# Optimization experiments

Hardware: AMD Instinct MI355X
Metric: run time of the kernel (lower is better)

The kernel has to match this reference:

```python
import jax, jax.numpy as jnp
import numpy as np

N, E, P, D = 100000, 800000, 100000, 128

def setup_inputs() -> dict:
    key = jax.random.key(0)
    ks = jax.random.split(key, 24)
    def w(k, i, o):
        return jax.random.normal(k, (i, o), jnp.float32) * (1.0 / np.sqrt(i))
    inp = {
        'x': jax.random.normal(ks[0], (N, D), jnp.float32),
        'src': jax.random.randint(ks[1], (E,), 0, N, jnp.int32),
        'dst': jax.random.randint(ks[2], (E,), 0, N, jnp.int32),
        'pos_src': jax.random.randint(ks[3], (P,), 0, N, jnp.int32),
        'pos_dst': jax.random.randint(ks[4], (P,), 0, N, jnp.int32),
        'neg_src': jax.random.randint(ks[5], (P,), 0, N, jnp.int32),
        'neg_dst': jax.random.randint(ks[6], (P,), 0, N, jnp.int32),
        # SAGEConv params: fc_self, fc_neigh (+bias) per layer
        'Ws0': w(ks[7], D, D), 'Wn0': w(ks[8], D, D), 'b0': jnp.zeros((D,), jnp.float32),
        'Ws1': w(ks[9], D, D), 'Wn1': w(ks[10], D, D), 'b1': jnp.zeros((D,), jnp.float32),
        'Ws2': w(ks[11], D, D), 'Wn2': w(ks[12], D, D), 'b2': jnp.zeros((D,), jnp.float32),
        # predictor MLP: D->D->D->2
        'Wp0': w(ks[13], D, D), 'bp0': jnp.zeros((D,), jnp.float32),
        'Wp1': w(ks[14], D, D), 'bp1': jnp.zeros((D,), jnp.float32),
        'Wp2': w(ks[15], D, 2), 'bp2': jnp.zeros((2,), jnp.float32),
    }
    return inp

def _sage_layer(h, src, dst, n, Ws, Wn, b, act):
    # mean aggregation over in-neighbors (gather -> segment_sum -> divide)
    msum = jax.ops.segment_sum(h[src], dst, num_segments=n)      # [N, D]
    deg = jax.ops.segment_sum(jnp.ones_like(dst, jnp.float32), dst, num_segments=n)
    h_neigh = msum / jnp.maximum(deg, 1.0)[:, None]
    out = h @ Ws + h_neigh @ Wn + b
    return jax.nn.relu(out) if act else out

def _predict(hs, hd, Wp0, bp0, Wp1, bp1, Wp2, bp2):
    z = hs * hd
    z = jax.nn.relu(z @ Wp0 + bp0)
    z = jax.nn.relu(z @ Wp1 + bp1)
    return jax.nn.softmax(z @ Wp2 + bp2, axis=1)[:, 1]

def reference(x, src, dst, pos_src, pos_dst, neg_src, neg_dst,
              Ws0, Wn0, b0, Ws1, Wn1, b1, Ws2, Wn2, b2,
              Wp0, bp0, Wp1, bp1, Wp2, bp2):
    n = x.shape[0]
    h = _sage_layer(x, src, dst, n, Ws0, Wn0, b0, True)
    h = _sage_layer(h, src, dst, n, Ws1, Wn1, b1, True)
    h = _sage_layer(h, src, dst, n, Ws2, Wn2, b2, False)
    pos = _predict(h[pos_src], h[pos_dst], Wp0, bp0, Wp1, bp1, Wp2, bp2)
    neg = _predict(h[neg_src], h[neg_dst], Wp0, bp0, Wp1, bp1, Wp2, bp2)
    return (pos, neg)
```

## Files before the change

### kernel.cpp

```cpp
#include <hip/hip_runtime.h>
#include <cstdint>
#include <cstddef>
#include <cmath>

#define D 128

typedef short bf16x8 __attribute__((ext_vector_type(8)));
typedef float f32x4 __attribute__((ext_vector_type(4)));

__device__ __forceinline__ ushort f2b(float f) {
  uint x = __float_as_uint(f);
  uint r = ((x >> 16) & 1u) + 0x7fffu;
  return (ushort)((x + r) >> 16);
}
__device__ __forceinline__ float b2f(ushort u) {
  return __uint_as_float(((uint)u) << 16);
}

__global__ void k_degree(const int* __restrict__ dst, int E, int* __restrict__ deg) {
  int e = blockIdx.x * blockDim.x + threadIdx.x;
  if (e < E) atomicAdd(&deg[dst[e]], 1);
}

#define SCAN_T 256
#define SCAN_E 4
#define SCAN_CHUNK (SCAN_T * SCAN_E)

__global__ void k_scan_partial(const int* __restrict__ deg, int n, int* __restrict__ part) {
  __shared__ int s[SCAN_T];
  int base = blockIdx.x * SCAN_CHUNK;
  int sum = 0;
  for (int i = 0; i < SCAN_E; ++i) {
    int idx = base + (int)threadIdx.x * SCAN_E + i;
    if (idx < n) sum += deg[idx];
  }
  s[threadIdx.x] = sum; __syncthreads();
  for (int ofs = SCAN_T / 2; ofs > 0; ofs >>= 1) {
    if ((int)threadIdx.x < ofs) s[threadIdx.x] += s[threadIdx.x + ofs];
    __syncthreads();
  }
  if (threadIdx.x == 0) part[blockIdx.x] = s[0];
}

__global__ void k_scan_part_ex(int* __restrict__ part, int nb) {
  __shared__ int s[1024];
  int v = ((int)threadIdx.x < nb) ? part[threadIdx.x] : 0;
  s[threadIdx.x] = v; __syncthreads();
  for (int ofs = 1; ofs < 1024; ofs <<= 1) {
    int t = ((int)threadIdx.x >= ofs) ? s[threadIdx.x - ofs] : 0;
    __syncthreads();
    s[threadIdx.x] += t;
    __syncthreads();
  }
  if ((int)threadIdx.x < nb) part[threadIdx.x] = s[threadIdx.x] - v;
}

__global__ void k_scan_final(const int* __restrict__ deg, int n, const int* __restrict__ part,
                             int* __restrict__ rowptr, int E) {
  __shared__ int s[SCAN_T];
  int base = blockIdx.x * SCAN_CHUNK;
  int v[SCAN_E]; int local = 0;
  for (int i = 0; i < SCAN_E; ++i) {
    int idx = base + (int)threadIdx.x * SCAN_E + i;
    v[i] = (idx < n) ? deg[idx] : 0;
    local += v[i];
  }
  s[threadIdx.x] = local; __syncthreads();
  for (int ofs = 1; ofs < SCAN_T; ofs <<= 1) {
    int t = ((int)threadIdx.x >= ofs) ? s[threadIdx.x - ofs] : 0;
    __syncthreads();
    s[threadIdx.x] += t;
    __syncthreads();
  }
  int run = part[blockIdx.x] + s[threadIdx.x] - local;
  for (int i = 0; i < SCAN_E; ++i) {
    int idx = base + (int)threadIdx.x * SCAN_E + i;
    if (idx < n) rowptr[idx] = run;
    run += v[i];
  }
  if (blockIdx.x == 0 && threadIdx.x == 0) rowptr[n] = E;
}

__global__ void k_fill(const int* __restrict__ src, const int* __restrict__ dst, int E,
                       int* __restrict__ cursor, int* __restrict__ csrc) {
  int e = blockIdx.x * blockDim.x + threadIdx.x;
  if (e < E) {
    int p = atomicAdd(&cursor[dst[e]], 1);
    csrc[p] = src[e];
  }
}

__global__ void k_conv_bf16(const float* __restrict__ in, ushort* __restrict__ out, int n8) {
  int i = blockIdx.x * 256 + threadIdx.x;
  if (i >= n8) return;
  float4 a = ((const float4*)in)[i * 2];
  float4 b = ((const float4*)in)[i * 2 + 1];
  ushort4 o0 = {f2b(a.x), f2b(a.y), f2b(a.z), f2b(a.w)};
  ushort4 o1 = {f2b(b.x), f2b(b.y), f2b(b.z), f2b(b.w)};
  ((ushort4*)out)[i * 2] = o0;
  ((ushort4*)out)[i * 2 + 1] = o1;
}

__global__ void k_packW(const float* __restrict__ W0, const float* __restrict__ W1,
                        ushort* __restrict__ out, int ksteps) {
  int o = blockIdx.x * 256 + threadIdx.x;
  int total = ksteps * 4096;
  if (o >= total) return;
  int j = o & 7, lane = (o >> 3) & 63, t = (o >> 9) & 7, ks = o >> 12;
  int k = ks * 32 + ((lane >> 4) * 8) + j;
  int n = t * 16 + (lane & 15);
  const float* W = (k < 128) ? W0 : W1;
  int kk = (k < 128) ? k : k - 128;
  out[o] = f2b(W[(size_t)kk * D + n]);
}

__global__ __launch_bounds__(256) void k_aggregate_b(const ushort* __restrict__ h,
    const int* __restrict__ rowptr, const int* __restrict__ csrc,
    ushort* __restrict__ hn, int N) {
  int wid = (int)((blockIdx.x * (size_t)blockDim.x + threadIdx.x) >> 6);
  int lane = threadIdx.x & 63;
  if (wid >= N) return;
  int grp = lane >> 4, sub = lane & 15;
  int beg = rowptr[wid], end = rowptr[wid + 1];
  const ushort* hb = h + sub * 8;
  float f[8] = {0.f, 0.f, 0.f, 0.f, 0.f, 0.f, 0.f, 0.f};
  int i = beg + grp;
  for (; i + 4 < end; i += 8) {
    int s0 = csrc[i], s1 = csrc[i + 4];
    bf16x8 v0 = *(const bf16x8*)(hb + (size_t)s0 * D);
    bf16x8 v1 = *(const bf16x8*)(hb + (size_t)s1 * D);
    #pragma unroll
    for (int j = 0; j < 8; ++j)
      f[j] += b2f((ushort)v0[j]) + b2f((ushort)v1[j]);
  }
  if (i < end) {
    int s0 = csrc[i];
    bf16x8 v0 = *(const bf16x8*)(hb + (size_t)s0 * D);
    #pragma unroll
    for (int j = 0; j < 8; ++j) f[j] += b2f((ushort)v0[j]);
  }
  #pragma unroll
  for (int j = 0; j < 8; ++j) {
    f[j] += __shfl_xor(f[j], 16);
    f[j] += __shfl_xor(f[j], 32);
  }
  if (grp == 0) {
    float inv = (end > beg) ? (1.0f / (float)(end - beg)) : 0.0f;
    bf16x8 o;
    #pragma unroll
    for (int j = 0; j < 8; ++j) o[j] = (short)f2b(f[j] * inv);
    *(bf16x8*)(hn + (size_t)wid * D + sub * 8) = o;
  }
}

__global__ __launch_bounds__(256) void k_gemm_mfma(
    const ushort* __restrict__ A, const ushort* __restrict__ An,
    const ushort* __restrict__ Bp, const float* __restrict__ bias,
    ushort* __restrict__ out, int N, int do_relu) {
  int tid = threadIdx.x;
  int wave = tid >> 6, lane = tid & 63;
  int m = lane & 15, kg = lane >> 4;
  int row0 = blockIdx.x * 64 + wave * 16;
  int ar = row0 + m; if (ar >= N) ar = N - 1;
  const ushort* a_self = A  + (size_t)ar * D + kg * 8;
  const ushort* a_nei  = An + (size_t)ar * D + kg * 8;
  f32x4 acc[8];
  #pragma unroll
  for (int t = 0; t < 8; ++t) acc[t] = f32x4{0.f, 0.f, 0.f, 0.f};
  #pragma unroll
  for (int ks = 0; ks < 8; ++ks) {
    const ushort* ap = (ks < 4) ? a_self : a_nei;
    bf16x8 af = *(const bf16x8*)(ap + (ks & 3) * 32);
    const ushort* bb = Bp + (size_t)ks * 4096 + lane * 8;
    #pragma unroll
    for (int t = 0; t < 8; ++t)
      acc[t] = __builtin_amdgcn_mfma_f32_16x16x32_bf16(af, *(const bf16x8*)(bb + t * 512), acc[t], 0, 0, 0);
  }
  #pragma unroll
  for (int t = 0; t < 8; ++t) {
    int c = t * 16 + m;
    float bv = bias[c];
    #pragma unroll
    for (int i = 0; i < 4; ++i) {
      int r = row0 + kg * 4 + i;
      float v = acc[t][i] + bv;
      if (do_relu) v = fmaxf(v, 0.f);
      if (r < N) out[(size_t)r * D + c] = f2b(v);
    }
  }
}

__global__ __launch_bounds__(256) void k_predict_mfma(
    const ushort* __restrict__ h, const int* __restrict__ sidx, const int* __restrict__ didx,
    const ushort* __restrict__ Bp0, const float* __restrict__ bp0,
    const ushort* __restrict__ Bp1, const float* __restrict__ bp1,
    const float* __restrict__ Wp2, const float* __restrict__ bp2,
    float* __restrict__ outp, int P) {
  __shared__ __align__(16) ushort z1p[4][2048];
  int tid = threadIdx.x;
  int wave = tid >> 6, lane = tid & 63;
  int m = lane & 15, kg = lane >> 4;
  int pair0 = blockIdx.x * 64 + wave * 16;
  int prow = pair0 + m; int pr = (prow < P) ? prow : P - 1;
  int si = sidx[pr], di = didx[pr];
  const ushort* hs = h + (size_t)si * D + kg * 8;
  const ushort* hd = h + (size_t)di * D + kg * 8;
  f32x4 acc[8];
  #pragma unroll
  for (int t = 0; t < 8; ++t) acc[t] = f32x4{0.f, 0.f, 0.f, 0.f};
  #pragma unroll
  for (int ks = 0; ks < 4; ++ks) {
    bf16x8 as8 = *(const bf16x8*)(hs + ks * 32);
    bf16x8 ad8 = *(const bf16x8*)(hd + ks * 32);
    bf16x8 af;
    #pragma unroll
    for (int j = 0; j < 8; ++j) {
      float p = b2f((ushort)as8[j]) * b2f((ushort)ad8[j]);
      af[j] = (short)f2b(p);
    }
    const ushort* bb = Bp0 + (size_t)ks * 4096 + lane * 8;
    #pragma unroll
    for (int t = 0; t < 8; ++t)
      acc[t] = __builtin_amdgcn_mfma_f32_16x16x32_bf16(af, *(const bf16x8*)(bb + t * 512), acc[t], 0, 0, 0);
  }
  ushort* zp = &z1p[wave][0];
  #pragma unroll
  for (int t = 0; t < 8; ++t) {
    int c = t * 16 + m;
    float bv = bp0[c];
    int ks2 = c >> 5, kg2 = (c >> 3) & 3, j2 = c & 7;
    #pragma unroll
    for (int i = 0; i < 4; ++i) {
      float v = fmaxf(acc[t][i] + bv, 0.f);
      int l2 = kg2 * 16 + kg * 4 + i;
      zp[(ks2 * 64 + l2) * 8 + j2] = f2b(v);
    }
  }
  __syncthreads();
  #pragma unroll
  for (int t = 0; t < 8; ++t) acc[t] = f32x4{0.f, 0.f, 0.f, 0.f};
  #pragma unroll
  for (int ks = 0; ks < 4; ++ks) {
    bf16x8 af = *(const bf16x8*)(zp + (ks * 64 + lane) * 8);
    const ushort* bb = Bp1 + (size_t)ks * 4096 + lane * 8;
    #pragma unroll
    for (int t = 0; t < 8; ++t)
      acc[t] = __builtin_amdgcn_mfma_f32_16x16x32_bf16(af, *(const bf16x8*)(bb + t * 512), acc[t], 0, 0, 0);
  }
  float p0[4] = {0.f, 0.f, 0.f, 0.f}, p1[4] = {0.f, 0.f, 0.f, 0.f};
  #pragma unroll
  for (int t = 0; t < 8; ++t) {
    int c = t * 16 + m;
    float bv = bp1[c];
    float wa = Wp2[(size_t)c * 2], wb = Wp2[(size_t)c * 2 + 1];
    #pragma unroll
    for (int i = 0; i < 4; ++i) {
      float z = fmaxf(acc[t][i] + bv, 0.f);
      p0[i] += z * wa;
      p1[i] += z * wb;
    }
  }
  #pragma unroll
  for (int msk = 1; msk <= 8; msk <<= 1) {
    #pragma unroll
    for (int i = 0; i < 4; ++i) {
      p0[i] += __shfl_xor(p0[i], msk);
      p1[i] += __shfl_xor(p1[i], msk);
    }
  }
  if (m == 0) {
    float c0 = bp2[0], c1 = bp2[1];
    #pragma unroll
    for (int i = 0; i < 4; ++i) {
      int r = pair0 + kg * 4 + i;
      if (r < P) {
        float l0 = p0[i] + c0, l1 = p1[i] + c1;
        outp[r] = 1.0f / (1.0f + expf(l0 - l1));
      }
    }
  }
}

extern "C" void kernel_launch(void* const* d_in, const int* in_sizes, int n_in,
                              void* d_out, int out_size, void* d_ws, size_t ws_size,
                              hipStream_t stream) {
  const float* x       = (const float*)d_in[0];
  const int*   src     = (const int*)d_in[1];
  const int*   dst     = (const int*)d_in[2];
  const int*   pos_src = (const int*)d_in[3];
  const int*   pos_dst = (const int*)d_in[4];
  const int*   neg_src = (const int*)d_in[5];
  const int*   neg_dst = (const int*)d_in[6];
  const float* Ws0 = (const float*)d_in[7],  *Wn0 = (const float*)d_in[8],  *b0 = (const float*)d_in[9];
  const float* Ws1 = (const float*)d_in[10], *Wn1 = (const float*)d_in[11], *b1 = (const float*)d_in[12];
  const float* Ws2 = (const float*)d_in[13], *Wn2 = (const float*)d_in[14], *b2 = (const float*)d_in[15];
  const float* Wp0 = (const float*)d_in[16], *bp0 = (const float*)d_in[17];
  const float* Wp1 = (const float*)d_in[18], *bp1 = (const float*)d_in[19];
  const float* Wp2 = (const float*)d_in[20], *bp2 = (const float*)d_in[21];
  const int N = in_sizes[0] / D;
  const int E = in_sizes[1];
  const int P = in_sizes[3];
  float* outp = (float*)d_out;

  char* ws = (char*)d_ws;
  size_t off = 0;
  auto alloc = [&](size_t bytes) -> void* {
    void* p = ws + off;
    off += (bytes + 255) & ~(size_t)255;
    return p;
  };
  ushort* xb    = (ushort*)alloc((size_t)N * D * 2);
  ushort* h1    = (ushort*)alloc((size_t)N * D * 2);
  ushort* h2    = (ushort*)alloc((size_t)N * D * 2);
  ushort* hn    = (ushort*)alloc((size_t)N * D * 2);
  ushort* BpL0  = (ushort*)alloc(256 * D * 2);
  ushort* BpL1  = (ushort*)alloc(256 * D * 2);
  ushort* BpL2  = (ushort*)alloc(256 * D * 2);
  ushort* BpP0  = (ushort*)alloc(128 * D * 2);
  ushort* BpP1  = (ushort*)alloc(128 * D * 2);
  int*    deg    = (int*)alloc((size_t)N * 4);
  int*    rowptr = (int*)alloc((size_t)(N + 1) * 4);
  int*    cursor = (int*)alloc((size_t)N * 4);
  int*    part   = (int*)alloc(4096);
  int*    csrc   = (int*)alloc((size_t)E * 4);
  (void)ws_size; (void)n_in; (void)out_size;

  hipMemsetAsync(deg, 0, (size_t)N * 4, stream);
  int eb = (E + 255) / 256;
  k_degree<<<eb, 256, 0, stream>>>(dst, E, deg);
  int nb = (N + SCAN_CHUNK - 1) / SCAN_CHUNK;
  k_scan_partial<<<nb, SCAN_T, 0, stream>>>(deg, N, part);
  k_scan_part_ex<<<1, 1024, 0, stream>>>(part, nb);
  k_scan_final<<<nb, SCAN_T, 0, stream>>>(deg, N, part, rowptr, E);
  hipMemcpyAsync(cursor, rowptr, (size_t)N * 4, hipMemcpyDeviceToDevice, stream);
  k_fill<<<eb, 256, 0, stream>>>(src, dst, E, cursor, csrc);

  int n8 = N * D / 8;
  k_conv_bf16<<<(n8 + 255) / 256, 256, 0, stream>>>(x, xb, n8);
  k_packW<<<(8 * 4096 + 255) / 256, 256, 0, stream>>>(Ws0, Wn0, BpL0, 8);
  k_packW<<<(8 * 4096 + 255) / 256, 256, 0, stream>>>(Ws1, Wn1, BpL1, 8);
  k_packW<<<(8 * 4096 + 255) / 256, 256, 0, stream>>>(Ws2, Wn2, BpL2, 8);
  k_packW<<<(4 * 4096 + 255) / 256, 256, 0, stream>>>(Wp0, Wp0, BpP0, 4);
  k_packW<<<(4 * 4096 + 255) / 256, 256, 0, stream>>>(Wp1, Wp1, BpP1, 4);

  int aggb = (int)(((size_t)N * 64 + 255) / 256);
  int gemb = (N + 63) / 64;
  k_aggregate_b<<<aggb, 256, 0, stream>>>(xb, rowptr, csrc, hn, N);
  k_gemm_mfma<<<gemb, 256, 0, stream>>>(xb, hn, BpL0, b0, h1, N, 1);
  k_aggregate_b<<<aggb, 256, 0, stream>>>(h1, rowptr, csrc, hn, N);
  k_gemm_mfma<<<gemb, 256, 0, stream>>>(h1, hn, BpL1, b1, h2, N, 1);
  k_aggregate_b<<<aggb, 256, 0, stream>>>(h2, rowptr, csrc, hn, N);
  k_gemm_mfma<<<gemb, 256, 0, stream>>>(h2, hn, BpL2, b2, xb, N, 0);
  int pb = (P + 63) / 64;
  k_predict_mfma<<<pb, 256, 0, stream>>>(xb, pos_src, pos_dst, BpP0, bp0, BpP1, bp1, Wp2, bp2, outp, P);
  k_predict_mfma<<<pb, 256, 0, stream>>>(xb, neg_src, neg_dst, BpP0, bp0, BpP1, bp1, Wp2, bp2, outp + P, P);
}
```

Baseline: 500.2 us.

## Fuse aggregation into SAGE GEMM, partition CSR build, merge pack and predict launches

Each SAGE layer now does its neighbor mean aggregation inside the GEMM kernel, staging the 16 mean rows per wave in shared memory. This removes the hn intermediate buffer and three extra launches. The degree and fill kernels are split into 8 destination-range partitions, with each block handling only one partition so atomics land in a narrower address range. Weight packing and the pos/neg predictions are each merged into a single launch. The costs are that every edge chunk is read 8 times during the CSR build, and the aggregation inside the fused kernel now runs at GEMM-block granularity, so occupancy and latency hiding may be lower.

```diff
diff --git a/kernel.cpp b/kernel.cpp
--- a/kernel.cpp
+++ b/kernel.cpp
@@ -17,9 +17,37 @@
   return __uint_as_float(((uint)u) << 16);
 }
 
-__global__ void k_degree(const int* __restrict__ dst, int E, int* __restrict__ deg) {
-  int e = blockIdx.x * blockDim.x + threadIdx.x;
-  if (e < E) atomicAdd(&deg[dst[e]], 1);
+__global__ __launch_bounds__(256) void k_degree_p(const int* __restrict__ dst, int E,
+    int* __restrict__ deg, float scale, int CE) {
+  int part = blockIdx.x & 7, chunk = blockIdx.x >> 3;
+  long base = (long)chunk * CE;
+  for (int i = threadIdx.x; i < CE; i += 256) {
+    long e = base + i;
+    if (e < E) {
+      int d = dst[e];
+      int p = (int)((float)d * scale); if (p > 7) p = 7;
+      if (p == part) atomicAdd(&deg[d], 1);
+    }
+  }
+}
+
+__global__ __launch_bounds__(256) void k_fill_p(const int* __restrict__ src,
+    const int* __restrict__ dst, int E, int* __restrict__ cursor,
+    int* __restrict__ csrc, float scale, int CE) {
+  int part = blockIdx.x & 7, chunk = blockIdx.x >> 3;
+  long base = (long)chunk * CE;
+  for (int i = threadIdx.x; i < CE; i += 256) {
+    long e = base + i;
+    if (e < E) {
+      int d = dst[e];
+      int p = (int)((float)d * scale); if (p > 7) p = 7;
+      if (p == part) {
+        int s = src[e];
+        int pos = atomicAdd(&cursor[d], 1);
+        csrc[pos] = s;
+      }
+    }
+  }
 }
 
 #define SCAN_T 256
@@ -81,15 +109,6 @@
   if (blockIdx.x == 0 && threadIdx.x == 0) rowptr[n] = E;
 }
 
-__global__ void k_fill(const int* __restrict__ src, const int* __restrict__ dst, int E,
-                       int* __restrict__ cursor, int* __restrict__ csrc) {
-  int e = blockIdx.x * blockDim.x + threadIdx.x;
-  if (e < E) {
-    int p = atomicAdd(&cursor[dst[e]], 1);
-    csrc[p] = src[e];
-  }
-}
-
 __global__ void k_conv_bf16(const float* __restrict__ in, ushort* __restrict__ out, int n8) {
   int i = blockIdx.x * 256 + threadIdx.x;
   if (i >= n8) return;
@@ -101,76 +120,82 @@
   ((ushort4*)out)[i * 2 + 1] = o1;
 }
 
-__global__ void k_packW(const float* __restrict__ W0, const float* __restrict__ W1,
-                        ushort* __restrict__ out, int ksteps) {
+__global__ void k_pack_all(
+    const float* __restrict__ Ws0, const float* __restrict__ Wn0,
+    const float* __restrict__ Ws1, const float* __restrict__ Wn1,
+    const float* __restrict__ Ws2, const float* __restrict__ Wn2,
+    const float* __restrict__ Wp0, const float* __restrict__ Wp1,
+    ushort* __restrict__ BpL0, ushort* __restrict__ BpL1, ushort* __restrict__ BpL2,
+    ushort* __restrict__ BpP0, ushort* __restrict__ BpP1) {
   int o = blockIdx.x * 256 + threadIdx.x;
-  int total = ksteps * 4096;
-  if (o >= total) return;
-  int j = o & 7, lane = (o >> 3) & 63, t = (o >> 9) & 7, ks = o >> 12;
+  const float *W0, *W1; ushort* out; int rel;
+  if (o < 32768)       { W0 = Ws0; W1 = Wn0; out = BpL0; rel = o; }
+  else if (o < 65536)  { W0 = Ws1; W1 = Wn1; out = BpL1; rel = o - 32768; }
+  else if (o < 98304)  { W0 = Ws2; W1 = Wn2; out = BpL2; rel = o - 65536; }
+  else if (o < 114688) { W0 = Wp0; W1 = Wp0; out = BpP0; rel = o - 98304; }
+  else                 { W0 = Wp1; W1 = Wp1; out = BpP1; rel = o - 114688; }
+  int j = rel & 7, lane = (rel >> 3) & 63, t = (rel >> 9) & 7, ks = rel >> 12;
   int k = ks * 32 + ((lane >> 4) * 8) + j;
   int n = t * 16 + (lane & 15);
   const float* W = (k < 128) ? W0 : W1;
   int kk = (k < 128) ? k : k - 128;
-  out[o] = f2b(W[(size_t)kk * D + n]);
-}
-
-__global__ __launch_bounds__(256) void k_aggregate_b(const ushort* __restrict__ h,
-    const int* __restrict__ rowptr, const int* __restrict__ csrc,
-    ushort* __restrict__ hn, int N) {
-  int wid = (int)((blockIdx.x * (size_t)blockDim.x + threadIdx.x) >> 6);
-  int lane = threadIdx.x & 63;
-  if (wid >= N) return;
-  int grp = lane >> 4, sub = lane & 15;
-  int beg = rowptr[wid], end = rowptr[wid + 1];
-  const ushort* hb = h + sub * 8;
-  float f[8] = {0.f, 0.f, 0.f, 0.f, 0.f, 0.f, 0.f, 0.f};
-  int i = beg + grp;
-  for (; i + 4 < end; i += 8) {
-    int s0 = csrc[i], s1 = csrc[i + 4];
-    bf16x8 v0 = *(const bf16x8*)(hb + (size_t)s0 * D);
-    bf16x8 v1 = *(const bf16x8*)(hb + (size_t)s1 * D);
-    #pragma unroll
-    for (int j = 0; j < 8; ++j)
-      f[j] += b2f((ushort)v0[j]) + b2f((ushort)v1[j]);
-  }
-  if (i < end) {
-    int s0 = csrc[i];
-    bf16x8 v0 = *(const bf16x8*)(hb + (size_t)s0 * D);
-    #pragma unroll
-    for (int j = 0; j < 8; ++j) f[j] += b2f((ushort)v0[j]);
-  }
-  #pragma unroll
-  for (int j = 0; j < 8; ++j) {
-    f[j] += __shfl_xor(f[j], 16);
-    f[j] += __shfl_xor(f[j], 32);
-  }
-  if (grp == 0) {
-    float inv = (end > beg) ? (1.0f / (float)(end - beg)) : 0.0f;
-    bf16x8 o;
-    #pragma unroll
-    for (int j = 0; j < 8; ++j) o[j] = (short)f2b(f[j] * inv);
-    *(bf16x8*)(hn + (size_t)wid * D + sub * 8) = o;
-  }
-}
-
-__global__ __launch_bounds__(256) void k_gemm_mfma(
-    const ushort* __restrict__ A, const ushort* __restrict__ An,
-    const ushort* __restrict__ Bp, const float* __restrict__ bias,
-    ushort* __restrict__ out, int N, int do_relu) {
-  int tid = threadIdx.x;
-  int wave = tid >> 6, lane = tid & 63;
+  out[rel] = f2b(W[(size_t)kk * D + n]);
+}
+
+#define SMS 136
+__global__ __launch_bounds__(256) void k_sage_fused(
+    const ushort* __restrict__ A, const int* __restrict__ rowptr,
+    const int* __restrict__ csrc, const ushort* __restrict__ Bp,
+    const float* __restrict__ bias, ushort* __restrict__ out, int N, int do_relu) {
+  __shared__ __align__(16) ushort smean[4][16][SMS];
+  int tid = threadIdx.x, wave = tid >> 6, lane = tid & 63;
   int m = lane & 15, kg = lane >> 4;
   int row0 = blockIdx.x * 64 + wave * 16;
+  int rp = 0;
+  { int idx = row0 + lane; if (lane < 17 && idx <= N) rp = rowptr[idx]; }
+  const ushort* hb = A + m * 8;
+  for (int t = 0; t < 16; ++t) {
+    int beg = __shfl(rp, t), end = __shfl(rp, t + 1);
+    if (end < beg) end = beg;
+    float f[8] = {0.f, 0.f, 0.f, 0.f, 0.f, 0.f, 0.f, 0.f};
+    int i = beg + kg;
+    for (; i + 4 < end; i += 8) {
+      int s0 = csrc[i], s1 = csrc[i + 4];
+      bf16x8 v0 = *(const bf16x8*)(hb + (size_t)s0 * D);
+      bf16x8 v1 = *(const bf16x8*)(hb + (size_t)s1 * D);
+      #pragma unroll
+      for (int j = 0; j < 8; ++j)
+        f[j] += b2f((ushort)v0[j]) + b2f((ushort)v1[j]);
+    }
+    if (i < end) {
+      int s0 = csrc[i];
+      bf16x8 v0 = *(const bf16x8*)(hb + (size_t)s0 * D);
+      #pragma unroll
+      for (int j = 0; j < 8; ++j) f[j] += b2f((ushort)v0[j]);
+    }
+    #pragma unroll
+    for (int j = 0; j < 8; ++j) {
+      f[j] += __shfl_xor(f[j], 16);
+      f[j] += __shfl_xor(f[j], 32);
+    }
+    if (kg == 0) {
+      float inv = (end > beg) ? (1.0f / (float)(end - beg)) : 0.0f;
+      bf16x8 o;
+      #pragma unroll
+      for (int j = 0; j < 8; ++j) o[j] = (short)f2b(f[j] * inv);
+      *(bf16x8*)&smean[wave][t][m * 8] = o;
+    }
+  }
+  __syncthreads();
   int ar = row0 + m; if (ar >= N) ar = N - 1;
-  const ushort* a_self = A  + (size_t)ar * D + kg * 8;
-  const ushort* a_nei  = An + (size_t)ar * D + kg * 8;
+  const ushort* a_self = A + (size_t)ar * D + kg * 8;
   f32x4 acc[8];
   #pragma unroll
   for (int t = 0; t < 8; ++t) acc[t] = f32x4{0.f, 0.f, 0.f, 0.f};
   #pragma unroll
   for (int ks = 0; ks < 8; ++ks) {
-    const ushort* ap = (ks < 4) ? a_self : a_nei;
-    bf16x8 af = *(const bf16x8*)(ap + (ks & 3) * 32);
+    bf16x8 af = (ks < 4) ? *(const bf16x8*)(a_self + ks * 32)
+                         : *(const bf16x8*)&smean[wave][m][(ks - 4) * 32 + kg * 8];
     const ushort* bb = Bp + (size_t)ks * 4096 + lane * 8;
     #pragma unroll
     for (int t = 0; t < 8; ++t)
@@ -191,16 +216,22 @@
 }
 
 __global__ __launch_bounds__(256) void k_predict_mfma(
-    const ushort* __restrict__ h, const int* __restrict__ sidx, const int* __restrict__ didx,
+    const ushort* __restrict__ h,
+    const int* __restrict__ ps, const int* __restrict__ pd,
+    const int* __restrict__ ns, const int* __restrict__ nd,
     const ushort* __restrict__ Bp0, const float* __restrict__ bp0,
     const ushort* __restrict__ Bp1, const float* __restrict__ bp1,
     const float* __restrict__ Wp2, const float* __restrict__ bp2,
-    float* __restrict__ outp, int P) {
+    float* __restrict__ outp, int P, int pb) {
   __shared__ __align__(16) ushort z1p[4][2048];
+  int bi = blockIdx.x;
+  const int* sidx; const int* didx; float* op;
+  if (bi >= pb) { sidx = ns; didx = nd; op = outp + P; bi -= pb; }
+  else          { sidx = ps; didx = pd; op = outp; }
   int tid = threadIdx.x;
   int wave = tid >> 6, lane = tid & 63;
   int m = lane & 15, kg = lane >> 4;
-  int pair0 = blockIdx.x * 64 + wave * 16;
+  int pair0 = bi * 64 + wave * 16;
   int prow = pair0 + m; int pr = (prow < P) ? prow : P - 1;
   int si = sidx[pr], di = didx[pr];
   const ushort* hs = h + (size_t)si * D + kg * 8;
@@ -275,7 +306,7 @@
       int r = pair0 + kg * 4 + i;
       if (r < P) {
         float l0 = p0[i] + c0, l1 = p1[i] + c1;
-        outp[r] = 1.0f / (1.0f + expf(l0 - l1));
+        op[r] = 1.0f / (1.0f + expf(l0 - l1));
       }
     }
   }
@@ -312,7 +343,6 @@
   ushort* xb    = (ushort*)alloc((size_t)N * D * 2);
   ushort* h1    = (ushort*)alloc((size_t)N * D * 2);
   ushort* h2    = (ushort*)alloc((size_t)N * D * 2);
-  ushort* hn    = (ushort*)alloc((size_t)N * D * 2);
   ushort* BpL0  = (ushort*)alloc(256 * D * 2);
   ushort* BpL1  = (ushort*)alloc(256 * D * 2);
   ushort* BpL2  = (ushort*)alloc(256 * D * 2);
@@ -325,33 +355,30 @@
   int*    csrc   = (int*)alloc((size_t)E * 4);
   (void)ws_size; (void)n_in; (void)out_size;
 
+  const float pscale = 8.0f / (float)N;
+  const int CB = 96;
+  const int CE = (E + CB - 1) / CB;
+
   hipMemsetAsync(deg, 0, (size_t)N * 4, stream);
-  int eb = (E + 255) / 256;
-  k_degree<<<eb, 256, 0, stream>>>(dst, E, deg);
+  k_degree_p<<<8 * CB, 256, 0, stream>>>(dst, E, deg, pscale, CE);
   int nb = (N + SCAN_CHUNK - 1) / SCAN_CHUNK;
   k_scan_partial<<<nb, SCAN_T, 0, stream>>>(deg, N, part);
   k_scan_part_ex<<<1, 1024, 0, stream>>>(part, nb);
   k_scan_final<<<nb, SCAN_T, 0, stream>>>(deg, N, part, rowptr, E);
   hipMemcpyAsync(cursor, rowptr, (size_t)N * 4, hipMemcpyDeviceToDevice, stream);
-  k_fill<<<eb, 256, 0, stream>>>(src, dst, E, cursor, csrc);
+  k_fill_p<<<8 * CB, 256, 0, stream>>>(src, dst, E, cursor, csrc, pscale, CE);
 
   int n8 = N * D / 8;
   k_conv_bf16<<<(n8 + 255) / 256, 256, 0, stream>>>(x, xb, n8);
-  k_packW<<<(8 * 4096 + 255) / 256, 256, 0, stream>>>(Ws0, Wn0, BpL0, 8);
-  k_packW<<<(8 * 4096 + 255) / 256, 256, 0, stream>>>(Ws1, Wn1, BpL1, 8);
-  k_packW<<<(8 * 4096 + 255) / 256, 256, 0, stream>>>(Ws2, Wn2, BpL2, 8);
-  k_packW<<<(4 * 4096 + 255) / 256, 256, 0, stream>>>(Wp0, Wp0, BpP0, 4);
-  k_packW<<<(4 * 4096 + 255) / 256, 256, 0, stream>>>(Wp1, Wp1, BpP1, 4);
-
-  int aggb = (int)(((size_t)N * 64 + 255) / 256);
+  k_pack_all<<<512, 256, 0, stream>>>(Ws0, Wn0, Ws1, Wn1, Ws2, Wn2, Wp0, Wp1,
+                                      BpL0, BpL1, BpL2, BpP0, BpP1);
+
   int gemb = (N + 63) / 64;
-  k_aggregate_b<<<aggb, 256, 0, stream>>>(xb, rowptr, csrc, hn, N);
-  k_gemm_mfma<<<gemb, 256, 0, stream>>>(xb, hn, BpL0, b0, h1, N, 1);
-  k_aggregate_b<<<aggb, 256, 0, stream>>>(h1, rowptr, csrc, hn, N);
-  k_gemm_mfma<<<gemb, 256, 0, stream>>>(h1, hn, BpL1, b1, h2, N, 1);
-  k_aggregate_b<<<aggb, 256, 0, stream>>>(h2, rowptr, csrc, hn, N);
-  k_gemm_mfma<<<gemb, 256, 0, stream>>>(h2, hn, BpL2, b2, xb, N, 0);
+  k_sage_fused<<<gemb, 256, 0, stream>>>(xb, rowptr, csrc, BpL0, b0, h1, N, 1);
+  k_sage_fused<<<gemb, 256, 0, stream>>>(h1, rowptr, csrc, BpL1, b1, h2, N, 1);
+  k_sage_fused<<<gemb, 256, 0, stream>>>(h2, rowptr, csrc, BpL2, b2, xb, N, 0);
+
   int pb = (P + 63) / 64;
-  k_predict_mfma<<<pb, 256, 0, stream>>>(xb, pos_src, pos_dst, BpP0, bp0, BpP1, bp1, Wp2, bp2, outp, P);
-  k_predict_mfma<<<pb, 256, 0, stream>>>(xb, neg_src, neg_dst, BpP0, bp0, BpP1, bp1, Wp2, bp2, outp + P, P);
-}
+  k_predict_mfma<<<2 * pb, 256, 0, stream>>>(xb, pos_src, pos_dst, neg_src, neg_dst,
+                                             BpP0, bp0, BpP1, bp1, Wp2, bp2, outp, P, pb);
+}
```

Result: no change. 498.0 us (-0.4%).
